# Performance work log

Hardware: AMD Instinct MI355X
Metric: run time of the kernel (lower is better)

## Reference

```python
import jax, jax.numpy as jnp
import numpy as np

V, D = 100000, 128
B, W, K = 16384, 10, 10


def setup_inputs() -> dict:
    key = jax.random.key(0)
    k1, k2, k3, k4, k5 = jax.random.split(key, 5)
    init_range = 0.5 / D
    return {
        "context": jax.random.randint(k1, (B, W), 0, V, dtype=jnp.int64 if jax.config.jax_enable_x64 else jnp.int32),
        "target": jax.random.randint(k2, (B,), 0, V, dtype=jnp.int64 if jax.config.jax_enable_x64 else jnp.int32),
        "noise": jax.random.randint(k3, (B, K), 0, V, dtype=jnp.int64 if jax.config.jax_enable_x64 else jnp.int32),
        "emb_w": jax.random.uniform(k4, (V, D), jnp.float32, -init_range, init_range),
        "ctx_w": jax.random.uniform(k5, (V, D), jnp.float32, -init_range, init_range),
    }


def reference(context, target, noise, emb_w, ctx_w):
    # Gather + mean-pool context embeddings: [B, W, D] -> [B, D]
    context_vec = ctx_w[context].mean(axis=1)
    # Target embeddings: [B, D]
    target_vec = emb_w[target]
    # Original does matmul(target_vec, context_vec.T).diag(); same math as row-wise dot.
    pos_score = jax.nn.log_sigmoid(jnp.einsum("bd,bd->b", target_vec, context_vec))  # [B]
    # Negative samples: [B, K, D] x [B, D] -> [B, K], then log-sigmoid and sum -> [B, 1]
    noise_vec = emb_w[noise]
    neg_score = jax.nn.log_sigmoid(jnp.einsum("bkd,bd->bk", noise_vec, context_vec)).sum(axis=1, keepdims=True)  # [B, 1]
    # Faithful to torch broadcasting bug: [B] + [B,1] -> [B,B], then mean.
    return -(pos_score[None, :] + neg_score).mean()
```

## Files before the change

kernel.cpp:

```cpp
#include <hip/hip_runtime.h>
#include <hip/hip_bf16.h>
#include <math.h>


#define CBOW_B 16384
#define CBOW_W 10
#define CBOW_K 10
#define CBOW_D 128
#define ROWS_PER_BLOCK 16
#define NBLOCKS (CBOW_B / ROWS_PER_BLOCK)

__device__ __forceinline__ float log_sigmoid(float x) {
    const float t = __expf(-fabsf(x));
    return fminf(x, 0.0f) - __logf(1.0f + t);
}

__device__ __forceinline__ float group_reduce_sum(float s) {
    s += __shfl_xor(s, 8, 64);
    s += __shfl_xor(s, 4, 64);
    s += __shfl_xor(s, 2, 64);
    s += __shfl_xor(s, 1, 64);
    return s;
}

__global__ __launch_bounds__(256) void cbow_main(
    const int* __restrict__ context,
    const int* __restrict__ target,
    const int* __restrict__ noise,
    const float* __restrict__ emb_w,
    const float* __restrict__ ctx_w,
    float* __restrict__ block_sums)
{
    const int wave = threadIdx.x >> 6;
    const int lane = threadIdx.x & 63;
    const int grp  = lane >> 4;
    const int sub  = lane & 15;
    const int b = blockIdx.x * ROWS_PER_BLOCK + wave * 4 + grp;

    const int elem = sub * 8;

    float c0x=0,c0y=0,c0z=0,c0w=0, c1x=0,c1y=0,c1z=0,c1w=0;
    #pragma unroll
    for (int w = 0; w < CBOW_W; ++w) {
        const int idx = context[b * CBOW_W + w];
        const float4* p = reinterpret_cast<const float4*>(
            &ctx_w[(long long)idx * CBOW_D + elem]);
        const float4 r0 = p[0];
        const float4 r1 = p[1];
        c0x += r0.x; c0y += r0.y; c0z += r0.z; c0w += r0.w;
        c1x += r1.x; c1y += r1.y; c1z += r1.z; c1w += r1.w;
    }
    const float inv = 1.0f / CBOW_W;
    c0x*=inv; c0y*=inv; c0z*=inv; c0w*=inv;
    c1x*=inv; c1y*=inv; c1z*=inv; c1w*=inv;

    float sum = 0.0f;
    #pragma unroll
    for (int k = 0; k < CBOW_K + 1; ++k) {
        const int idx = (k == 0) ? target[b] : noise[b * CBOW_K + (k - 1)];
        const float4* p = reinterpret_cast<const float4*>(
            &emb_w[(long long)idx * CBOW_D + elem]);
        const float4 r0 = p[0];
        const float4 r1 = p[1];
        float part = c0x*r0.x + c0y*r0.y + c0z*r0.z + c0w*r0.w
                   + c1x*r1.x + c1y*r1.y + c1z*r1.z + c1w*r1.w;
        const float dot = group_reduce_sum(part);
        sum += log_sigmoid(dot);
    }

    sum += __shfl_xor(sum, 16, 64);
    sum += __shfl_xor(sum, 32, 64);

    __shared__ float wsum[4];
    if (lane == 0) wsum[wave] = sum;
    __syncthreads();
    if (threadIdx.x == 0) {
        float s = 0.0f;
        #pragma unroll
        for (int i = 0; i < 4; ++i) s += wsum[i];
        block_sums[blockIdx.x] = s;
    }
}

__global__ __launch_bounds__(256) void cbow_finish(
    const float* __restrict__ block_sums, float* __restrict__ out)
{
    __shared__ double sh[256];
    double s = 0.0;
    for (int i = threadIdx.x; i < NBLOCKS; i += 256) s += (double)block_sums[i];
    sh[threadIdx.x] = s;
    __syncthreads();
    #pragma unroll
    for (int stride = 128; stride >= 1; stride >>= 1) {
        if (threadIdx.x < stride) sh[threadIdx.x] += sh[threadIdx.x + stride];
        __syncthreads();
    }
    if (threadIdx.x == 0) {
        out[0] = (float)(-sh[0] / (double)CBOW_B);
    }
}

extern "C" void kernel_launch(void* const* d_in, const int* in_sizes, int n_in,
                              void* d_out, int out_size, void* d_ws, size_t ws_size,
                              hipStream_t stream) {
    const int*   context = (const int*)d_in[0];
    const int*   target  = (const int*)d_in[1];
    const int*   noise   = (const int*)d_in[2];
    const float* emb_w   = (const float*)d_in[3];
    const float* ctx_w   = (const float*)d_in[4];
    float*       out     = (float*)d_out;
    float*       block_sums = (float*)d_ws;

    cbow_main<<<NBLOCKS, 256, 0, stream>>>(context, target, noise, emb_w, ctx_w,
                                           block_sums);
    cbow_finish<<<1, 256, 0, stream>>>(block_sums, out);
}
```

Measured before the change: 32.11 us.

## Use 32 lanes per row with float4 loads and vectorized index loads

Each batch row is now handled by 32 lanes that each load one float4, instead of 16 lanes loading two float4s. Blocks cover 8 rows instead of 16, which doubles the grid. Context and noise indices are read as int2 pairs up front, and addressing uses 32-bit unsigned arithmetic. The goal is more memory-level parallelism and cheaper address math for the gather-bound workload, at the cost of one more shuffle step per dot product and twice as many partial sums for the finish kernel.

```diff
diff --git a/kernel.cpp b/kernel.cpp
--- a/kernel.cpp
+++ b/kernel.cpp
@@ -7,20 +7,12 @@
 #define CBOW_W 10
 #define CBOW_K 10
 #define CBOW_D 128
-#define ROWS_PER_BLOCK 16
+#define ROWS_PER_BLOCK 8
 #define NBLOCKS (CBOW_B / ROWS_PER_BLOCK)
 
 __device__ __forceinline__ float log_sigmoid(float x) {
     const float t = __expf(-fabsf(x));
     return fminf(x, 0.0f) - __logf(1.0f + t);
-}
-
-__device__ __forceinline__ float group_reduce_sum(float s) {
-    s += __shfl_xor(s, 8, 64);
-    s += __shfl_xor(s, 4, 64);
-    s += __shfl_xor(s, 2, 64);
-    s += __shfl_xor(s, 1, 64);
-    return s;
 }
 
 __global__ __launch_bounds__(256) void cbow_main(
@@ -33,42 +25,46 @@
 {
     const int wave = threadIdx.x >> 6;
     const int lane = threadIdx.x & 63;
-    const int grp  = lane >> 4;
-    const int sub  = lane & 15;
-    const int b = blockIdx.x * ROWS_PER_BLOCK + wave * 4 + grp;
+    const int grp  = lane >> 5;
+    const int sub  = lane & 31;
+    const int b = blockIdx.x * ROWS_PER_BLOCK + wave * 2 + grp;
+    const unsigned elem = sub * 4u;
 
-    const int elem = sub * 8;
+    const int2* cI = reinterpret_cast<const int2*>(&context[b * CBOW_W]);
+    const int2 c01 = cI[0], c23 = cI[1], c45 = cI[2], c67 = cI[3], c89 = cI[4];
+    const int2* nI = reinterpret_cast<const int2*>(&noise[b * CBOW_K]);
+    const int2 n01 = nI[0], n23 = nI[1], n45 = nI[2], n67 = nI[3], n89 = nI[4];
+    const int tgt = target[b];
 
-    float c0x=0,c0y=0,c0z=0,c0w=0, c1x=0,c1y=0,c1z=0,c1w=0;
-    #pragma unroll
-    for (int w = 0; w < CBOW_W; ++w) {
-        const int idx = context[b * CBOW_W + w];
-        const float4* p = reinterpret_cast<const float4*>(
-            &ctx_w[(long long)idx * CBOW_D + elem]);
-        const float4 r0 = p[0];
-        const float4 r1 = p[1];
-        c0x += r0.x; c0y += r0.y; c0z += r0.z; c0w += r0.w;
-        c1x += r1.x; c1y += r1.y; c1z += r1.z; c1w += r1.w;
-    }
+    float cx = 0, cy = 0, cz = 0, cw = 0;
+    #define CBOW_ACC(IDX) {                                                    \
+        const float4 r = *reinterpret_cast<const float4*>(                     \
+            ctx_w + ((unsigned)(IDX) * (unsigned)CBOW_D + elem));              \
+        cx += r.x; cy += r.y; cz += r.z; cw += r.w; }
+    CBOW_ACC(c01.x) CBOW_ACC(c01.y) CBOW_ACC(c23.x) CBOW_ACC(c23.y)
+    CBOW_ACC(c45.x) CBOW_ACC(c45.y) CBOW_ACC(c67.x) CBOW_ACC(c67.y)
+    CBOW_ACC(c89.x) CBOW_ACC(c89.y)
+    #undef CBOW_ACC
     const float inv = 1.0f / CBOW_W;
-    c0x*=inv; c0y*=inv; c0z*=inv; c0w*=inv;
-    c1x*=inv; c1y*=inv; c1z*=inv; c1w*=inv;
+    cx *= inv; cy *= inv; cz *= inv; cw *= inv;
 
     float sum = 0.0f;
-    #pragma unroll
-    for (int k = 0; k < CBOW_K + 1; ++k) {
-        const int idx = (k == 0) ? target[b] : noise[b * CBOW_K + (k - 1)];
-        const float4* p = reinterpret_cast<const float4*>(
-            &emb_w[(long long)idx * CBOW_D + elem]);
-        const float4 r0 = p[0];
-        const float4 r1 = p[1];
-        float part = c0x*r0.x + c0y*r0.y + c0z*r0.z + c0w*r0.w
-                   + c1x*r1.x + c1y*r1.y + c1z*r1.z + c1w*r1.w;
-        const float dot = group_reduce_sum(part);
-        sum += log_sigmoid(dot);
-    }
+    #define CBOW_DOT(IDX) {                                                    \
+        const float4 r = *reinterpret_cast<const float4*>(                     \
+            emb_w + ((unsigned)(IDX) * (unsigned)CBOW_D + elem));              \
+        float p = cx * r.x + cy * r.y + cz * r.z + cw * r.w;                   \
+        p += __shfl_xor(p, 1, 64);                                             \
+        p += __shfl_xor(p, 2, 64);                                             \
+        p += __shfl_xor(p, 4, 64);                                             \
+        p += __shfl_xor(p, 8, 64);                                             \
+        p += __shfl_xor(p, 16, 64);                                            \
+        sum += log_sigmoid(p); }
+    CBOW_DOT(tgt)
+    CBOW_DOT(n01.x) CBOW_DOT(n01.y) CBOW_DOT(n23.x) CBOW_DOT(n23.y)
+    CBOW_DOT(n45.x) CBOW_DOT(n45.y) CBOW_DOT(n67.x) CBOW_DOT(n67.y)
+    CBOW_DOT(n89.x) CBOW_DOT(n89.y)
+    #undef CBOW_DOT
 
-    sum += __shfl_xor(sum, 16, 64);
     sum += __shfl_xor(sum, 32, 64);
 
     __shared__ float wsum[4];
```

Result: slower. 34.93 us (+8.8%).
